# Kernel tuning notes

Measured on AMD Instinct MI355X. Metric: run time of the kernel, lower is better.

Reference implementation:

```python
import jax, jax.numpy as jnp
import numpy as np

H = 16      # num_heads
D = 64      # nhid (per-head dim)
SL, BS = 1024, 64
DM = 1024   # keys_dim == query_dim == values_dim

def setup_inputs() -> dict:
    key = jax.random.key(0)
    k1, k2, k3, k4, k5 = jax.random.split(key, 5)
    return {
        "query":  jax.random.normal(k1, (BS, DM), dtype=jnp.float32),
        "keys":   jax.random.normal(k2, (SL, BS, DM), dtype=jnp.float32),
        "values": jax.random.normal(k3, (SL, BS, DM), dtype=jnp.float32),
        "Wq":     jax.random.normal(k4, (H * D, DM), dtype=jnp.float32) * 0.02,
        "Wk":     jax.random.normal(k5, (H * D, DM), dtype=jnp.float32) * 0.02,
    }

def reference(query, keys, values, Wq, Wk):
    bs = query.shape[0]
    sl = keys.shape[0]
    scale = jnp.asarray(np.sqrt(D), dtype=query.dtype)
    # projections (note: original module applies keys_linear to values -- a bug we replicate)
    qp = (query @ Wq.T).reshape(bs, H, D)                 # [bs, H, D]
    kp = (keys @ Wk.T).reshape(sl, bs, H, D)              # [sl, bs, H, D]
    vp = (values @ Wk.T).reshape(sl, bs, H, D)            # [sl, bs, H, D]
    # per-head scaled dot-product scores, softmax over the sequence axis (dim 0)
    scores = jnp.einsum('bhd,sbhd->sbh', qp, kp) / scale  # [sl, bs, H]
    attn = jax.nn.softmax(scores, axis=0)
    out = jnp.einsum('sbh,sbhd->bhd', attn, vp)           # [bs, H, D]
    return out.reshape(bs, H * D)
```

## Files before the change

kernel.cpp:

```cpp
#include <hip/hip_runtime.h>
#include <cstddef>
#include <cstdint>

#define NH 16
#define HD 64
#define SLEN 1024
#define NB 64
#define DMODEL 1024

#define DOT4_ACC(acc, k, q) \
  acc = fmaf((k).x, (q).x, fmaf((k).y, (q).y, fmaf((k).z, (q).z, fmaf((k).w, (q).w, (acc)))))

#define FMA4_BCAST(accv, qv, w0_, w1_, w2_, w3_) do { \
  (accv).x = fmaf((qv).x, (w0_).x, fmaf((qv).y, (w1_).x, fmaf((qv).z, (w2_).x, fmaf((qv).w, (w3_).x, (accv).x)))); \
  (accv).y = fmaf((qv).x, (w0_).y, fmaf((qv).y, (w1_).y, fmaf((qv).z, (w2_).y, fmaf((qv).w, (w3_).y, (accv).y)))); \
  (accv).z = fmaf((qv).x, (w0_).z, fmaf((qv).y, (w1_).z, fmaf((qv).z, (w2_).z, fmaf((qv).w, (w3_).z, (accv).z)))); \
  (accv).w = fmaf((qv).x, (w0_).w, fmaf((qv).y, (w1_).w, fmaf((qv).z, (w2_).w, fmaf((qv).w, (w3_).w, (accv).w)))); \
} while (0)

__device__ __forceinline__ float wred_sum(float v) {
#pragma unroll
  for (int off = 32; off; off >>= 1) v += __shfl_xor(v, off, 64);
  return v;
}

__device__ __forceinline__ void gload16(const float* g, float* lds_base) {
  __builtin_amdgcn_global_load_lds(
      (const __attribute__((address_space(1))) void*)g,
      (__attribute__((address_space(3))) void*)lds_base, 16, 0, 0);
}

__global__ __launch_bounds__(256) void k0_qp(const float* __restrict__ query,
                                             const float* __restrict__ Wq,
                                             float* __restrict__ qp) {
  const int tid = threadIdx.x;
  const int w = tid >> 6, l = tid & 63;
  const int j = blockIdx.x * 4 + w;
  const float4* wr = reinterpret_cast<const float4*>(Wq + (size_t)j * DMODEL) + l * 4;
  const float4 w0 = wr[0], w1 = wr[1], w2 = wr[2], w3 = wr[3];
  for (int b = 0; b < NB; ++b) {
    const float4* qr = reinterpret_cast<const float4*>(query + (size_t)b * DMODEL) + l * 4;
    float4 q0 = qr[0], q1 = qr[1], q2 = qr[2], q3 = qr[3];
    float s = 0.f;
    DOT4_ACC(s, w0, q0); DOT4_ACC(s, w1, q1); DOT4_ACC(s, w2, q2); DOT4_ACC(s, w3, q3);
    s = wred_sum(s);
    if (l == 0) qp[(size_t)b * DMODEL + j] = s;
  }
}

__global__ __launch_bounds__(256) void k1_qt(const float* __restrict__ qp,
                                             const float* __restrict__ Wk,
                                             float* __restrict__ qt) {
  __shared__ __align__(16) float qpl[8][HD];
  const int h = blockIdx.x & 15;
  const int b0 = (blockIdx.x >> 4) * 8;
  const int tid = threadIdx.x;
  for (int f = tid; f < 8 * HD; f += 256) {
    int bi = f >> 6, d = f & 63;
    qpl[bi][d] = qp[(size_t)(b0 + bi) * DMODEL + h * HD + d];
  }
  __syncthreads();
  const int m4 = tid * 4;
  float4 acc[8];
#pragma unroll
  for (int i = 0; i < 8; ++i) acc[i] = make_float4(0.f, 0.f, 0.f, 0.f);
  const float* wbase = Wk + (size_t)(h * HD) * DMODEL + m4;
  for (int d = 0; d < HD; d += 4) {
    float4 wk0 = *reinterpret_cast<const float4*>(wbase + (size_t)(d + 0) * DMODEL);
    float4 wk1 = *reinterpret_cast<const float4*>(wbase + (size_t)(d + 1) * DMODEL);
    float4 wk2 = *reinterpret_cast<const float4*>(wbase + (size_t)(d + 2) * DMODEL);
    float4 wk3 = *reinterpret_cast<const float4*>(wbase + (size_t)(d + 3) * DMODEL);
#pragma unroll
    for (int bi = 0; bi < 8; ++bi) {
      float4 q = *reinterpret_cast<const float4*>(&qpl[bi][d]);
      FMA4_BCAST(acc[bi], q, wk0, wk1, wk2, wk3);
    }
  }
#pragma unroll
  for (int bi = 0; bi < 8; ++bi)
    *reinterpret_cast<float4*>(qt + ((size_t)(b0 + bi) * NH + h) * DMODEL + m4) = acc[bi];
}

__global__ __launch_bounds__(128) void k2_scores(const float* __restrict__ keys,
                                                 const float* __restrict__ qt,
                                                 float* __restrict__ scp) {
  __shared__ __align__(16) float kb[2][128 * 16];
  __shared__ __align__(16) float qb[2][NH * 16];
  const int b  = blockIdx.x & 63;
  const int st = (blockIdx.x >> 6) & 7;
  const int mh = blockIdx.x >> 9;
  const int tid = threadIdx.x, w = tid >> 6, l = tid & 63;
  const int hg = l & 3;
  const int sg = l >> 2;
  const int s0 = st * 128;
  const size_t rowstride = (size_t)NB * DMODEL;
  const float* kbase = keys + ((size_t)s0 * NB + b) * DMODEL + mh * 512;
  const float* qbase = qt + (size_t)b * NH * DMODEL + mh * 512;
  const int srow  = l >> 2;
  const int sslot = (l & 3) ^ (srow & 3);
  const int qh = l >> 2, qj = l & 3;

#define K2_STAGE(buf_, ch_) do {                                              \
    _Pragma("unroll")                                                         \
    for (int i_ = 0; i_ < 4; ++i_) {                                          \
      const int u_ = w * 4 + i_;                                              \
      const int row_ = u_ * 16 + srow;                                        \
      gload16(kbase + (size_t)row_ * rowstride + (ch_) * 16 + sslot * 4,      \
              &kb[buf_][u_ * 256]);                                           \
    }                                                                         \
    if (w == 0)                                                               \
      gload16(qbase + (size_t)qh * DMODEL + (ch_) * 16 + qj * 4,              \
              &qb[buf_][0]);                                                  \
  } while (0)

  float acc[4][NH];
#pragma unroll
  for (int si = 0; si < 4; ++si)
#pragma unroll
    for (int hh = 0; hh < NH; ++hh) acc[si][hh] = 0.f;
  const int sl0 = w * 64 + sg;

  K2_STAGE(0, 0);
  __syncthreads();
  for (int ch = 0; ch < 32; ++ch) {
    const int buf = ch & 1;
    if (ch + 1 < 32) K2_STAGE(buf ^ 1, ch + 1);
    float4 kv[4];
#pragma unroll
    for (int si = 0; si < 4; ++si) {
      const int s = sl0 + si * 16;
      kv[si] = *reinterpret_cast<const float4*>(&kb[buf][s * 16 + ((hg ^ (s & 3)) << 2)]);
    }
#pragma unroll
    for (int hh = 0; hh < NH; ++hh) {
      float4 q = *reinterpret_cast<const float4*>(&qb[buf][hh * 16 + hg * 4]);
      DOT4_ACC(acc[0][hh], kv[0], q);
      DOT4_ACC(acc[1][hh], kv[1], q);
      DOT4_ACC(acc[2][hh], kv[2], q);
      DOT4_ACC(acc[3][hh], kv[3], q);
    }
    __syncthreads();
  }
#undef K2_STAGE
#pragma unroll
  for (int si = 0; si < 4; ++si)
#pragma unroll
    for (int hh = 0; hh < NH; ++hh) {
      acc[si][hh] += __shfl_xor(acc[si][hh], 1, 64);
      acc[si][hh] += __shfl_xor(acc[si][hh], 2, 64);
    }
  const float scale = 0.125f;
  float* plane = scp + (size_t)mh * NB * NH * SLEN;
#pragma unroll
  for (int j = 0; j < 4; ++j) {
#pragma unroll
    for (int si = 0; si < 4; ++si) {
      float r = hg == 0 ? acc[si][j] : hg == 1 ? acc[si][4 + j]
              : hg == 2 ? acc[si][8 + j] : acc[si][12 + j];
      plane[((size_t)b * NH + hg * 4 + j) * SLEN + s0 + sl0 + si * 16] = r * scale;
    }
  }
}

__global__ __launch_bounds__(256) void k_sm(float* __restrict__ sc0,
                                            const float* __restrict__ sc1) {
  __shared__ float red[8];
  const int tid = threadIdx.x, w = tid >> 6, l = tid & 63;
  float* p0 = sc0 + (size_t)blockIdx.x * SLEN;
  const float* p1 = sc1 + (size_t)blockIdx.x * SLEN;
  float4 xa = reinterpret_cast<const float4*>(p0)[tid];
  float4 xb = reinterpret_cast<const float4*>(p1)[tid];
  float4 x = make_float4(xa.x + xb.x, xa.y + xb.y, xa.z + xb.z, xa.w + xb.w);
  float mx = fmaxf(fmaxf(x.x, x.y), fmaxf(x.z, x.w));
#pragma unroll
  for (int off = 32; off; off >>= 1) mx = fmaxf(mx, __shfl_xor(mx, off, 64));
  if (l == 0) red[w] = mx;
  __syncthreads();
  mx = fmaxf(fmaxf(red[0], red[1]), fmaxf(red[2], red[3]));
  float4 e;
  e.x = __expf(x.x - mx); e.y = __expf(x.y - mx);
  e.z = __expf(x.z - mx); e.w = __expf(x.w - mx);
  float sum = e.x + e.y + e.z + e.w;
  sum = wred_sum(sum);
  if (l == 0) red[4 + w] = sum;
  __syncthreads();
  sum = red[4] + red[5] + red[6] + red[7];
  const float inv = 1.f / sum;
  e.x *= inv; e.y *= inv; e.z *= inv; e.w *= inv;
  reinterpret_cast<float4*>(p0)[tid] = e;
}

template <int NCH>
__global__ __launch_bounds__(256) void k3_cpart(const float* __restrict__ values,
                                                const float* __restrict__ attn,
                                                float* __restrict__ cp) {
  constexpr int SC = SLEN / NCH;
  __shared__ __align__(16) float vb[2][4][DMODEL];
  __shared__ __align__(16) float al[NH][SC];
  const int b = blockIdx.x & 63;
  const int ch = blockIdx.x >> 6;
  const int s0 = ch * SC;
  const int tid = threadIdx.x, w = tid >> 6, l = tid & 63;
  for (int f = tid; f < NH * (SC / 4); f += 256) {
    int hh = f / (SC / 4), c4 = (f % (SC / 4)) * 4;
    *reinterpret_cast<float4*>(&al[hh][c4]) = *reinterpret_cast<const float4*>(
        attn + ((size_t)b * NH + hh) * SLEN + s0 + c4);
  }
  const int m4 = tid * 4;
  float4 acc[NH];
#pragma unroll
  for (int i = 0; i < NH; ++i) acc[i] = make_float4(0.f, 0.f, 0.f, 0.f);
  const size_t rowstride = (size_t)NB * DMODEL;
  const float* vbase = values + ((size_t)s0 * NB + b) * DMODEL;

#define K3_STAGE(buf_, g_) do {                                               \
    const float* rg_ = vbase + (size_t)((g_) * 4 + w) * rowstride;            \
    _Pragma("unroll")                                                         \
    for (int j_ = 0; j_ < 4; ++j_)                                            \
      gload16(rg_ + j_ * 256 + l * 4, &vb[buf_][w][j_ * 256]);                \
  } while (0)

  K3_STAGE(0, 0);
  __syncthreads();
  for (int g = 0; g < SC / 4; ++g) {
    const int buf = g & 1;
    if (g + 1 < SC / 4) K3_STAGE(buf ^ 1, g + 1);
    float4 v0 = *reinterpret_cast<const float4*>(&vb[buf][0][m4]);
    float4 v1 = *reinterpret_cast<const float4*>(&vb[buf][1][m4]);
    float4 v2 = *reinterpret_cast<const float4*>(&vb[buf][2][m4]);
    float4 v3 = *reinterpret_cast<const float4*>(&vb[buf][3][m4]);
#pragma unroll
    for (int hh = 0; hh < NH; ++hh) {
      float4 av = *reinterpret_cast<const float4*>(&al[hh][g * 4]);
      FMA4_BCAST(acc[hh], av, v0, v1, v2, v3);
    }
    __syncthreads();
  }
#undef K3_STAGE
#pragma unroll
  for (int hh = 0; hh < NH; ++hh)
    *reinterpret_cast<float4*>(cp + (((size_t)ch * NB + b) * NH + hh) * DMODEL + m4) = acc[hh];
}

template <int NCH>
__global__ __launch_bounds__(256) void k4_out(const float* __restrict__ cp,
                                              const float* __restrict__ Wk,
                                              float* __restrict__ out) {
  __shared__ __align__(16) float cl[4 * DMODEL];
  const int h = blockIdx.x & 15;
  const int b0 = (blockIdx.x >> 4) * 4;
  const int tid = threadIdx.x, w = tid >> 6, l = tid & 63;
  for (int f = tid; f < 4 * DMODEL / 4; f += 256) {
    int bi = f >> 8, m4 = (f & 255) * 4;
    float4 s = make_float4(0.f, 0.f, 0.f, 0.f);
#pragma unroll
    for (int ch = 0; ch < NCH; ++ch) {
      float4 t = *reinterpret_cast<const float4*>(
          cp + (((size_t)ch * NB + b0 + bi) * NH + h) * DMODEL + m4);
      s.x += t.x; s.y += t.y; s.z += t.z; s.w += t.w;
    }
    *reinterpret_cast<float4*>(&cl[bi * DMODEL + m4]) = s;
  }
  __syncthreads();
  float4 c[4][4];
#pragma unroll
  for (int bi = 0; bi < 4; ++bi)
#pragma unroll
    for (int k = 0; k < 4; ++k)
      c[bi][k] = *reinterpret_cast<const float4*>(&cl[bi * DMODEL + l * 16 + k * 4]);
  for (int jj = 0; jj < 16; ++jj) {
    const int d = w * 16 + jj;
    const float4* wr = reinterpret_cast<const float4*>(Wk + (size_t)(h * HD + d) * DMODEL) + l * 4;
    const float4 w0 = wr[0], w1 = wr[1], w2 = wr[2], w3 = wr[3];
#pragma unroll
    for (int bi = 0; bi < 4; ++bi) {
      float s = 0.f;
      DOT4_ACC(s, w0, c[bi][0]); DOT4_ACC(s, w1, c[bi][1]);
      DOT4_ACC(s, w2, c[bi][2]); DOT4_ACC(s, w3, c[bi][3]);
      s = wred_sum(s);
      if (l == 0) out[(size_t)(b0 + bi) * (NH * HD) + h * HD + d] = s;
    }
  }
}

extern "C" void kernel_launch(void* const* d_in, const int* in_sizes, int n_in,
                              void* d_out, int out_size, void* d_ws, size_t ws_size,
                              hipStream_t stream) {
  const float* query  = (const float*)d_in[0];
  const float* keys   = (const float*)d_in[1];
  const float* values = (const float*)d_in[2];
  const float* Wq     = (const float*)d_in[3];
  const float* Wk     = (const float*)d_in[4];
  float* out = (float*)d_out;

  float* W   = (float*)d_ws;
  float* qp  = W;
  float* qt  = qp + (size_t)NB * DMODEL;
  float* sc0 = qt + (size_t)NB * NH * DMODEL;
  float* sc1 = sc0 + (size_t)NB * NH * SLEN;
  float* cp  = sc1 + (size_t)NB * NH * SLEN;

  const size_t base_floats = (size_t)NB * DMODEL + (size_t)NB * NH * DMODEL
                           + 2 * (size_t)NB * NH * SLEN;

  k0_qp<<<256, 256, 0, stream>>>(query, Wq, qp);
  k1_qt<<<128, 256, 0, stream>>>(qp, Wk, qt);
  k2_scores<<<1024, 128, 0, stream>>>(keys, qt, sc0);
  k_sm<<<NB * NH, 256, 0, stream>>>(sc0, sc1);

  const size_t chunk_floats = (size_t)NB * NH * DMODEL;
  if (ws_size >= (base_floats + 16 * chunk_floats) * sizeof(float)) {
    k3_cpart<16><<<16 * NB, 256, 0, stream>>>(values, sc0, cp);
    k4_out<16><<<NH * (NB / 4), 256, 0, stream>>>(cp, Wk, out);
  } else if (ws_size >= (base_floats + 8 * chunk_floats) * sizeof(float)) {
    k3_cpart<8><<<8 * NB, 256, 0, stream>>>(values, sc0, cp);
    k4_out<8><<<NH * (NB / 4), 256, 0, stream>>>(cp, Wk, out);
  } else {
    k3_cpart<4><<<4 * NB, 256, 0, stream>>>(values, sc0, cp);
    k4_out<4><<<NH * (NB / 4), 256, 0, stream>>>(cp, Wk, out);
  }
}
```

Measured before the change: 250.2 us.

## Retile score kernel so each wave handles four heads over wider chunks

The keys-by-query score kernel now gives each 256-thread block 64 sequence rows, loads 64-float chunks per stage with an XOR swizzle, and assigns four heads to each wave instead of all sixteen to every thread. This cuts per-thread accumulators from 64 to 16 and doubles the grid, aiming for more occupancy and fewer stage iterations. In exchange each key row in shared memory is now read by all four waves, and each block keeps a larger shared-memory footprint.

```diff
diff --git a/kernel.cpp b/kernel.cpp
--- a/kernel.cpp
+++ b/kernel.cpp
@@ -81,63 +81,72 @@
     *reinterpret_cast<float4*>(qt + ((size_t)(b0 + bi) * NH + h) * DMODEL + m4) = acc[bi];
 }
 
-__global__ __launch_bounds__(128) void k2_scores(const float* __restrict__ keys,
+__global__ __launch_bounds__(256) void k2_scores(const float* __restrict__ keys,
                                                  const float* __restrict__ qt,
                                                  float* __restrict__ scp) {
-  __shared__ __align__(16) float kb[2][128 * 16];
-  __shared__ __align__(16) float qb[2][NH * 16];
+  __shared__ __align__(16) float kb[2][64 * 64];
+  __shared__ __align__(16) float qb[2][NH * 64];
   const int b  = blockIdx.x & 63;
-  const int st = (blockIdx.x >> 6) & 7;
-  const int mh = blockIdx.x >> 9;
+  const int st = (blockIdx.x >> 6) & 15;
+  const int mh = blockIdx.x >> 10;
   const int tid = threadIdx.x, w = tid >> 6, l = tid & 63;
   const int hg = l & 3;
   const int sg = l >> 2;
-  const int s0 = st * 128;
+  const int s0 = st * 64;
   const size_t rowstride = (size_t)NB * DMODEL;
   const float* kbase = keys + ((size_t)s0 * NB + b) * DMODEL + mh * 512;
   const float* qbase = qt + (size_t)b * NH * DMODEL + mh * 512;
-  const int srow  = l >> 2;
-  const int sslot = (l & 3) ^ (srow & 3);
-  const int qh = l >> 2, qj = l & 3;
-
-#define K2_STAGE(buf_, ch_) do {                                              \
-    _Pragma("unroll")                                                         \
-    for (int i_ = 0; i_ < 4; ++i_) {                                          \
-      const int u_ = w * 4 + i_;                                              \
-      const int row_ = u_ * 16 + srow;                                        \
-      gload16(kbase + (size_t)row_ * rowstride + (ch_) * 16 + sslot * 4,      \
-              &kb[buf_][u_ * 256]);                                           \
-    }                                                                         \
-    if (w == 0)                                                               \
-      gload16(qbase + (size_t)qh * DMODEL + (ch_) * 16 + qj * 4,              \
-              &qb[buf_][0]);                                                  \
+  const int srow_lo = l >> 4;
+  const int sslot   = l & 15;
+  const int qh = w * 4 + (l >> 4);
+
+#define K2_STAGE(buf_, ch_) do {                                               \
+    _Pragma("unroll")                                                          \
+    for (int i_ = 0; i_ < 4; ++i_) {                                           \
+      const int row_ = i_ * 16 + w * 4 + srow_lo;                              \
+      gload16(kbase + (size_t)row_ * rowstride + (ch_) * 64 +                  \
+                  ((sslot ^ (row_ & 7)) << 2),                                 \
+              &kb[buf_][(i_ * 16 + w * 4) * 64]);                              \
+    }                                                                          \
+    gload16(qbase + (size_t)qh * DMODEL + (ch_) * 64 + (sslot << 2),           \
+            &qb[buf_][w * 4 * 64]);                                            \
   } while (0)
 
-  float acc[4][NH];
+  float acc[4][4];
 #pragma unroll
   for (int si = 0; si < 4; ++si)
 #pragma unroll
-    for (int hh = 0; hh < NH; ++hh) acc[si][hh] = 0.f;
-  const int sl0 = w * 64 + sg;
+    for (int hh = 0; hh < 4; ++hh) acc[si][hh] = 0.f;
 
   K2_STAGE(0, 0);
   __syncthreads();
-  for (int ch = 0; ch < 32; ++ch) {
+  for (int ch = 0; ch < 8; ++ch) {
     const int buf = ch & 1;
-    if (ch + 1 < 32) K2_STAGE(buf ^ 1, ch + 1);
-    float4 kv[4];
+    if (ch + 1 < 8) K2_STAGE(buf ^ 1, ch + 1);
+    float4 kv[4][4];
 #pragma unroll
     for (int si = 0; si < 4; ++si) {
-      const int s = sl0 + si * 16;
-      kv[si] = *reinterpret_cast<const float4*>(&kb[buf][s * 16 + ((hg ^ (s & 3)) << 2)]);
-    }
-#pragma unroll
-    for (int hh = 0; hh < NH; ++hh) {
-      float4 q = *reinterpret_cast<const float4*>(&qb[buf][hh * 16 + hg * 4]);
-      DOT4_ACC(acc[0][hh], kv[0], q);
-      DOT4_ACC(acc[1][hh], kv[1], q);
-      DOT4_ACC(acc[2][hh], kv[2], q);
-      DOT4_ACC(acc[3][hh], kv[3], q);
+      const int row = si * 16 + sg;
+      const int sw = (row & 7) << 2;
+#pragma unroll
+      for (int j = 0; j < 4; ++j)
+        kv[si][j] = *reinterpret_cast<const float4*>(
+            &kb[buf][row * 64 + ((hg * 4 + 16 * j) ^ sw)]);
+    }
+#pragma unroll
+    for (int hh = 0; hh < 4; ++hh) {
+      const float* qrow = &qb[buf][(w * 4 + hh) * 64 + hg * 4];
+      float4 q0 = *reinterpret_cast<const float4*>(qrow);
+      float4 q1 = *reinterpret_cast<const float4*>(qrow + 16);
+      float4 q2 = *reinterpret_cast<const float4*>(qrow + 32);
+      float4 q3 = *reinterpret_cast<const float4*>(qrow + 48);
+#pragma unroll
+      for (int si = 0; si < 4; ++si) {
+        DOT4_ACC(acc[si][hh], kv[si][0], q0);
+        DOT4_ACC(acc[si][hh], kv[si][1], q1);
+        DOT4_ACC(acc[si][hh], kv[si][2], q2);
+        DOT4_ACC(acc[si][hh], kv[si][3], q3);
+      }
     }
     __syncthreads();
   }
@@ -145,20 +154,17 @@
 #pragma unroll
   for (int si = 0; si < 4; ++si)
 #pragma unroll
-    for (int hh = 0; hh < NH; ++hh) {
+    for (int hh = 0; hh < 4; ++hh) {
       acc[si][hh] += __shfl_xor(acc[si][hh], 1, 64);
       acc[si][hh] += __shfl_xor(acc[si][hh], 2, 64);
     }
   const float scale = 0.125f;
   float* plane = scp + (size_t)mh * NB * NH * SLEN;
 #pragma unroll
-  for (int j = 0; j < 4; ++j) {
-#pragma unroll
-    for (int si = 0; si < 4; ++si) {
-      float r = hg == 0 ? acc[si][j] : hg == 1 ? acc[si][4 + j]
-              : hg == 2 ? acc[si][8 + j] : acc[si][12 + j];
-      plane[((size_t)b * NH + hg * 4 + j) * SLEN + s0 + sl0 + si * 16] = r * scale;
-    }
+  for (int si = 0; si < 4; ++si) {
+    float r = hg == 0 ? acc[si][0] : hg == 1 ? acc[si][1]
+            : hg == 2 ? acc[si][2] : acc[si][3];
+    plane[((size_t)b * NH + w * 4 + hg) * SLEN + s0 + si * 16 + sg] = r * scale;
   }
 }
 
@@ -305,7 +311,7 @@
 
   k0_qp<<<256, 256, 0, stream>>>(query, Wq, qp);
   k1_qt<<<128, 256, 0, stream>>>(qp, Wk, qt);
-  k2_scores<<<1024, 128, 0, stream>>>(keys, qt, sc0);
+  k2_scores<<<2048, 256, 0, stream>>>(keys, qt, sc0);
   k_sm<<<NB * NH, 256, 0, stream>>>(sc0, sc1);
 
   const size_t chunk_floats = (size_t)NB * NH * DMODEL;
```

Result: faster. 244.5 us (-2.2%).
